# Kernel tuning notes

Measured on AMD Instinct MI355X. Metric: run time of the kernel, lower is better.

## Reference

```python
import jax, jax.numpy as jnp
import numpy as np

M, IN, OUT = 8192, 4096, 4096
XOR_MASK = (1 << 3) | (1 << 7)  # 0x88: flips sign bit of each packed nibble


def _dequant_int4(weight_packed, weight_scales):
    """Decode packed int4 weights (offset-binary nibbles) to scaled float.

    weight_packed: [OUT, IN//2] int32, each byte holds two nibbles (v+8).
    Low nibble -> even input column, high nibble -> odd input column.
    """
    w = jnp.bitwise_xor(weight_packed, XOR_MASK)  # offset-binary -> two's complement nibbles
    low = jnp.bitwise_and(w, 0xF)
    high = jnp.bitwise_and(jnp.right_shift(w, 4), 0xF)
    low = jnp.where(low >= 8, low - 16, low)    # signed int4 in [-8, 7]
    high = jnp.where(high >= 8, high - 16, high)
    # interleave nibbles: [OUT, IN//2, 2] -> [OUT, IN]
    deq = jnp.stack([low, high], axis=-1).reshape(weight_packed.shape[0], -1)
    return deq.astype(weight_scales.dtype) * weight_scales[:, None]  # [OUT, IN]


def setup_inputs() -> dict:
    key = jax.random.key(0)
    k1, k2, k3, k4 = jax.random.split(key, 4)
    x = jax.random.normal(k1, (M, IN), dtype=jnp.float32)
    weight_packed = jax.random.randint(k2, (OUT, IN // 2), 0, 256, dtype=jnp.int32)
    weight_scales = jax.random.uniform(k3, (OUT,), dtype=jnp.float32) * 0.02 + 1e-3
    bias = jax.random.normal(k4, (OUT,), dtype=jnp.float32)
    return {"x": x, "weight_packed": weight_packed,
            "weight_scales": weight_scales, "bias": bias}


def reference(x, weight_packed, weight_scales, bias):
    # w4a16 forward: dequantize int4 weights per output row, then GEMM + bias.
    w = _dequant_int4(weight_packed, weight_scales)  # [OUT, IN]
    return jnp.dot(x, w.T) + bias  # [M, OUT]
```

## Files before the change

kernel.cpp:

```cpp
#include <hip/hip_runtime.h>
#include <cstdint>
#include <cstddef>

#define M_DIM 8192
#define K_DIM 4096
#define N_DIM 4096

typedef unsigned short u16;
typedef __bf16 bf16x8 __attribute__((ext_vector_type(8)));
typedef u16 u16x8 __attribute__((ext_vector_type(8)));
typedef float f32x4 __attribute__((ext_vector_type(4)));

__device__ __forceinline__ u16 f2bf_rne(float f) {
  uint32_t u = __builtin_bit_cast(uint32_t, f);
  return (u16)((u + 0x7FFFu + ((u >> 16) & 1u)) >> 16);
}
__device__ __forceinline__ u16 i2bf(int i) {
  return (u16)(__builtin_bit_cast(uint32_t, (float)i) >> 16);
}

#define XBLKS 16384
#define WBLKS 8192

__global__ __launch_bounds__(256) void prep(const float* __restrict__ x,
                                            const int* __restrict__ wp,
                                            u16* __restrict__ xb,
                                            u16* __restrict__ wb) {
  const int b = blockIdx.x;
  if (b < XBLKS) {
    size_t t = (size_t)b * 256 + threadIdx.x;
    const float4* xp = (const float4*)x;
    float4 a = xp[2 * t];
    float4 c = xp[2 * t + 1];
    u16x8 r;
    r[0] = f2bf_rne(a.x); r[1] = f2bf_rne(a.y); r[2] = f2bf_rne(a.z); r[3] = f2bf_rne(a.w);
    r[4] = f2bf_rne(c.x); r[5] = f2bf_rne(c.y); r[6] = f2bf_rne(c.z); r[7] = f2bf_rne(c.w);
    ((u16x8*)xb)[t] = r;
  } else {
    size_t t = (size_t)(b - XBLKS) * 256 + threadIdx.x;
    int4 p = ((const int4*)wp)[t];
    u16x8 r;
    int v;
    v = p.x ^ 0x88; r[0] = i2bf((v << 28) >> 28); r[1] = i2bf((v << 24) >> 28);
    v = p.y ^ 0x88; r[2] = i2bf((v << 28) >> 28); r[3] = i2bf((v << 24) >> 28);
    v = p.z ^ 0x88; r[4] = i2bf((v << 28) >> 28); r[5] = i2bf((v << 24) >> 28);
    v = p.w ^ 0x88; r[6] = i2bf((v << 28) >> 28); r[7] = i2bf((v << 24) >> 28);
    ((u16x8*)wb)[t] = r;
  }
}

__global__ __launch_bounds__(256, 2) void gemm_bt_w4a16(
    const u16* __restrict__ A,
    const u16* __restrict__ B,
    const float* __restrict__ scales,
    const float* __restrict__ bias,
    float* __restrict__ C) {
  __shared__ u16 sA[128 * 64];
  __shared__ u16 sB[128 * 64];

  const int tid = threadIdx.x;
  const int lane = tid & 63;
  const int wave = tid >> 6;
  const int m0 = blockIdx.y * 128;
  const int n0 = blockIdx.x * 128;
  const int wm = (wave & 1) * 64;
  const int wn = (wave >> 1) * 64;
  const int lrow = lane & 15;
  const int quad = lane >> 4;

  f32x4 acc[4][4] = {};

  const int srow = tid >> 3;
  const int key = srow & 7;
  const int schunk = ((tid & 7) ^ key) * 8;
  const u16* ga = A + (size_t)(m0 + srow) * K_DIM + schunk;
  const u16* gb = B + (size_t)(n0 + srow) * K_DIM + schunk;

  for (int kb = 0; kb < K_DIM; kb += 64) {
    __syncthreads();
#pragma unroll
    for (int r = 0; r < 4; ++r) {
      __builtin_amdgcn_global_load_lds(
          (const __attribute__((address_space(1))) void*)(ga + (size_t)(r * 32) * K_DIM + kb),
          (__attribute__((address_space(3))) void*)((char*)sA + wave * 1024 + r * 4096),
          16, 0, 0);
    }
#pragma unroll
    for (int r = 0; r < 4; ++r) {
      __builtin_amdgcn_global_load_lds(
          (const __attribute__((address_space(1))) void*)(gb + (size_t)(r * 32) * K_DIM + kb),
          (__attribute__((address_space(3))) void*)((char*)sB + wave * 1024 + r * 4096),
          16, 0, 0);
    }
    __syncthreads();

#pragma unroll
    for (int s = 0; s < 2; ++s) {
      u16x8 af[4], bfr[4];
#pragma unroll
      for (int i = 0; i < 4; ++i)
        af[i] = *(const u16x8*)(sA + (wm + i * 16 + lrow) * 64 +
                                ((s * 4 + quad) ^ (lrow & 7)) * 8);
#pragma unroll
      for (int j = 0; j < 4; ++j)
        bfr[j] = *(const u16x8*)(sB + (wn + j * 16 + lrow) * 64 +
                                 ((s * 4 + quad) ^ (lrow & 7)) * 8);
#pragma unroll
      for (int i = 0; i < 4; ++i)
#pragma unroll
        for (int j = 0; j < 4; ++j)
          acc[i][j] = __builtin_amdgcn_mfma_f32_16x16x32_bf16(
              __builtin_bit_cast(bf16x8, af[i]),
              __builtin_bit_cast(bf16x8, bfr[j]), acc[i][j], 0, 0, 0);
    }
  }

#pragma unroll
  for (int j = 0; j < 4; ++j) {
    const int n = n0 + wn + j * 16 + lrow;
    const float sc = scales[n];
    const float bi = bias[n];
#pragma unroll
    for (int i = 0; i < 4; ++i) {
#pragma unroll
      for (int r = 0; r < 4; ++r) {
        const int m = m0 + wm + i * 16 + quad * 4 + r;
        C[(size_t)m * N_DIM + n] = acc[i][j][r] * sc + bi;
      }
    }
  }
}

__global__ __launch_bounds__(256) void fallback_w4a16(
    const float* __restrict__ x, const int* __restrict__ wp,
    const float* __restrict__ scales, const float* __restrict__ bias,
    float* __restrict__ out) {
  const int n = blockIdx.x * 256 + threadIdx.x;
  const int m = blockIdx.y;
  const float* xr = x + (size_t)m * K_DIM;
  const int* wr = wp + (size_t)n * (K_DIM / 2);
  float acc = 0.f;
  for (int j = 0; j < K_DIM / 2; ++j) {
    int w = wr[j] ^ 0x88;
    float lo = (float)((w << 28) >> 28);
    float hi = (float)((w << 24) >> 28);
    acc += xr[2 * j] * lo + xr[2 * j + 1] * hi;
  }
  out[(size_t)m * N_DIM + n] = acc * scales[n] + bias[n];
}

extern "C" void kernel_launch(void* const* d_in, const int* in_sizes, int n_in,
                              void* d_out, int out_size, void* d_ws, size_t ws_size,
                              hipStream_t stream) {
  const float* x = (const float*)d_in[0];
  const int* wp = (const int*)d_in[1];
  const float* sc = (const float*)d_in[2];
  const float* bi = (const float*)d_in[3];
  float* out = (float*)d_out;

  const size_t xb_elems = (size_t)M_DIM * K_DIM;
  const size_t wb_elems = (size_t)N_DIM * K_DIM;
  const size_t need = (xb_elems + wb_elems) * sizeof(u16);

  if (ws_size >= need) {
    u16* xb = (u16*)d_ws;
    u16* wb = xb + xb_elems;
    prep<<<XBLKS + WBLKS, 256, 0, stream>>>(x, wp, xb, wb);
    gemm_bt_w4a16<<<dim3(N_DIM / 128, M_DIM / 128), 256, 0, stream>>>(xb, wb, sc, bi, out);
  } else {
    fallback_w4a16<<<dim3(N_DIM / 256, M_DIM), 256, 0, stream>>>(x, wp, sc, bi, out);
  }
}
```

Measured before the change: 475.2 us.

## Enlarge GEMM tile to 256x256 with 8 waves and double-buffered LDS

```diff
diff --git a/kernel.cpp b/kernel.cpp
--- a/kernel.cpp
+++ b/kernel.cpp
@@ -49,70 +49,85 @@
   }
 }
 
-__global__ __launch_bounds__(256, 2) void gemm_bt_w4a16(
+__global__ __launch_bounds__(512, 2) void gemm_bt_w4a16(
     const u16* __restrict__ A,
     const u16* __restrict__ B,
     const float* __restrict__ scales,
     const float* __restrict__ bias,
     float* __restrict__ C) {
-  __shared__ u16 sA[128 * 64];
-  __shared__ u16 sB[128 * 64];
+  __shared__ u16 sA[2][256 * 64];
+  __shared__ u16 sB[2][256 * 64];
 
   const int tid = threadIdx.x;
   const int lane = tid & 63;
   const int wave = tid >> 6;
-  const int m0 = blockIdx.y * 128;
-  const int n0 = blockIdx.x * 128;
-  const int wm = (wave & 1) * 64;
-  const int wn = (wave >> 1) * 64;
+  const int m0 = blockIdx.y * 256;
+  const int n0 = blockIdx.x * 256;
+  const int wm = (wave >> 2) * 128;
+  const int wn = (wave & 3) * 64;
   const int lrow = lane & 15;
   const int quad = lane >> 4;
 
-  f32x4 acc[4][4] = {};
+  f32x4 acc[8][4] = {};
 
   const int srow = tid >> 3;
-  const int key = srow & 7;
-  const int schunk = ((tid & 7) ^ key) * 8;
+  const int schunk = ((tid & 7) ^ (srow & 7)) * 8;
   const u16* ga = A + (size_t)(m0 + srow) * K_DIM + schunk;
   const u16* gb = B + (size_t)(n0 + srow) * K_DIM + schunk;
+  const int ldsoff = wave * 1024;
 
-  for (int kb = 0; kb < K_DIM; kb += 64) {
-    __syncthreads();
+  auto stage = [&](int buf, int kb) {
 #pragma unroll
-    for (int r = 0; r < 4; ++r) {
+    for (int r = 0; r < 4; ++r)
       __builtin_amdgcn_global_load_lds(
-          (const __attribute__((address_space(1))) void*)(ga + (size_t)(r * 32) * K_DIM + kb),
-          (__attribute__((address_space(3))) void*)((char*)sA + wave * 1024 + r * 4096),
+          (const __attribute__((address_space(1))) void*)(ga + (size_t)(r * 64) * K_DIM + kb),
+          (__attribute__((address_space(3))) void*)((char*)sA[buf] + r * 8192 + ldsoff),
           16, 0, 0);
-    }
 #pragma unroll
-    for (int r = 0; r < 4; ++r) {
+    for (int r = 0; r < 4; ++r)
       __builtin_amdgcn_global_load_lds(
-          (const __attribute__((address_space(1))) void*)(gb + (size_t)(r * 32) * K_DIM + kb),
-          (__attribute__((address_space(3))) void*)((char*)sB + wave * 1024 + r * 4096),
+          (const __attribute__((address_space(1))) void*)(gb + (size_t)(r * 64) * K_DIM + kb),
+          (__attribute__((address_space(3))) void*)((char*)sB[buf] + r * 8192 + ldsoff),
           16, 0, 0);
-    }
-    __syncthreads();
+  };
 
+  auto compute = [&](int buf) {
+    const u16* bA = sA[buf];
+    const u16* bB = sB[buf];
 #pragma unroll
     for (int s = 0; s < 2; ++s) {
-      u16x8 af[4], bfr[4];
+      const int kc = ((s * 4 + quad) ^ (lrow & 7)) * 8;
+      u16x8 af[8], bfr[4];
 #pragma unroll
-      for (int i = 0; i < 4; ++i)
-        af[i] = *(const u16x8*)(sA + (wm + i * 16 + lrow) * 64 +
-                                ((s * 4 + quad) ^ (lrow & 7)) * 8);
+      for (int i = 0; i < 8; ++i)
+        af[i] = *(const u16x8*)(bA + (wm + i * 16 + lrow) * 64 + kc);
 #pragma unroll
       for (int j = 0; j < 4; ++j)
-        bfr[j] = *(const u16x8*)(sB + (wn + j * 16 + lrow) * 64 +
-                                 ((s * 4 + quad) ^ (lrow & 7)) * 8);
+        bfr[j] = *(const u16x8*)(bB + (wn + j * 16 + lrow) * 64 + kc);
+      __builtin_amdgcn_s_setprio(1);
 #pragma unroll
-      for (int i = 0; i < 4; ++i)
+      for (int i = 0; i < 8; ++i)
 #pragma unroll
         for (int j = 0; j < 4; ++j)
           acc[i][j] = __builtin_amdgcn_mfma_f32_16x16x32_bf16(
               __builtin_bit_cast(bf16x8, af[i]),
               __builtin_bit_cast(bf16x8, bfr[j]), acc[i][j], 0, 0, 0);
+      __builtin_amdgcn_s_setprio(0);
     }
+  };
+
+  stage(0, 0);
+  __syncthreads();
+
+#pragma unroll 1
+  for (int it = 0; it < 32; ++it) {
+    const int kb = it * 128;
+    stage(1, kb + 64);
+    compute(0);
+    __syncthreads();
+    if (it < 31) stage(0, kb + 128);
+    compute(1);
+    __syncthreads();
   }
 
 #pragma unroll
@@ -121,12 +136,12 @@
     const float sc = scales[n];
     const float bi = bias[n];
 #pragma unroll
-    for (int i = 0; i < 4; ++i) {
+    for (int i = 0; i < 8; ++i) {
+      const int m = m0 + wm + i * 16 + quad * 4;
+      float* cp = &C[(size_t)m * N_DIM + n];
 #pragma unroll
-      for (int r = 0; r < 4; ++r) {
-        const int m = m0 + wm + i * 16 + quad * 4 + r;
-        C[(size_t)m * N_DIM + n] = acc[i][j][r] * sc + bi;
-      }
+      for (int r = 0; r < 4; ++r)
+        cp[(size_t)r * N_DIM] = acc[i][j][r] * sc + bi;
     }
   }
 }
@@ -166,7 +181,7 @@
     u16* xb = (u16*)d_ws;
     u16* wb = xb + xb_elems;
     prep<<<XBLKS + WBLKS, 256, 0, stream>>>(x, wp, xb, wb);
-    gemm_bt_w4a16<<<dim3(N_DIM / 128, M_DIM / 128), 256, 0, stream>>>(xb, wb, sc, bi, out);
+    gemm_bt_w4a16<<<dim3(N_DIM / 256, M_DIM / 256), 512, 0, stream>>>(xb, wb, sc, bi, out);
   } else {
     fallback_w4a16<<<dim3(N_DIM / 256, M_DIM), 256, 0, stream>>>(x, wp, sc, bi, out);
   }
```

Result: no change. 476.2 us (+0.2%).
